# Kernel tuning notes

Measured on AMD Instinct MI355X. Metric: run time of the kernel, lower is better.

## Reference

```python
import jax, jax.numpy as jnp
import numpy as np

N, E, D_NLP, D_EMB = 100000, 500000, 768, 128


def setup_inputs() -> dict:
    key = jax.random.key(0)
    ks = jax.random.split(key, 6)
    z = jax.random.normal(ks[0], (N, D_EMB), jnp.float32)
    z0 = jax.random.normal(ks[1], (N, D_NLP), jnp.float32)
    edge_index = jax.random.randint(ks[2], (2, E), 0, N)
    w0 = jax.random.normal(ks[3], (D_EMB, D_NLP), jnp.float32) / np.sqrt(D_NLP)
    prelu_a = jnp.full((1,), 0.25, jnp.float32)  # torch PReLU default init
    w1 = jax.random.normal(ks[4], (1, 3 * D_EMB), jnp.float32) / np.sqrt(3 * D_EMB)
    b1 = jnp.zeros((1,), jnp.float32)
    return {"z": z, "z0": z0, "edge_index": edge_index, "w0": w0,
            "prelu_a": prelu_a, "w1": w1, "b1": b1}


def reference(z, z0, edge_index, w0, prelu_a, w1, b1):
    # qid = elementwise max of the two endpoint rows, shifted to start at 0
    qid = jnp.max(edge_index[0:2], axis=0)
    qid = qid - qid.min()
    # lin0 (no bias) + PReLU with scalar slope
    h = z0[qid] @ w0.T                       # [E, D_EMB]
    x0 = jnp.where(h >= 0, h, prelu_a[0] * h)
    emb1 = z[edge_index[0]]                  # [E, D_EMB]
    emb2 = z[edge_index[1]]                  # [E, D_EMB]
    # lin1(concat([emb1, emb2, x0])) == sum of three matvecs; avoids a [E, 3*D] concat
    w1a, w1b, w1c = w1[0, :D_EMB], w1[0, D_EMB:2 * D_EMB], w1[0, 2 * D_EMB:]
    out = emb1 @ w1a + emb2 @ w1b + x0 @ w1c + b1[0]
    return out  # [E]
```

## Files before the change

kernel.cpp:

```cpp
#include <hip/hip_runtime.h>
#include <hip/hip_bf16.h>
#include <stdint.h>

#define D_EMB 128
#define D_NLP 768
#define BM 64
#define BK 64
#define NKC (D_NLP / BK)

typedef __attribute__((ext_vector_type(8))) short bf16x8;
typedef __attribute__((ext_vector_type(4))) float f32x4;
typedef __attribute__((ext_vector_type(8))) unsigned short u16x8;

__device__ __forceinline__ unsigned short f2bf(float f) {
  unsigned u = __builtin_bit_cast(unsigned, f);
  u += 0x7fffu + ((u >> 16) & 1u);
  return (unsigned short)(u >> 16);
}

__global__ void kw(const float* __restrict__ w0, unsigned short* __restrict__ w0s,
                   int* __restrict__ mn) {
  if (blockIdx.x == 0 && threadIdx.x == 0) mn[0] = 0x7fffffff;
  int t = blockIdx.x * 256 + threadIdx.x;
  if (t >= (D_EMB * D_NLP) / 8) return;
  int u = t & 7, row = (t >> 3) & 127, kc = t >> 10;
  const float4* src = (const float4*)(w0 + (size_t)row * D_NLP + kc * BK + ((u ^ (row & 7)) * 8));
  float4 v0 = src[0], v1 = src[1];
  u16x8 o;
  o[0] = f2bf(v0.x); o[1] = f2bf(v0.y); o[2] = f2bf(v0.z); o[3] = f2bf(v0.w);
  o[4] = f2bf(v1.x); o[5] = f2bf(v1.y); o[6] = f2bf(v1.z); o[7] = f2bf(v1.w);
  *(u16x8*)(w0s + (size_t)t * 8) = o;
}

__global__ void km(const int* __restrict__ ei, int E, int* __restrict__ mn) {
  int t = blockIdx.x * blockDim.x + threadIdx.x;
  int stride = gridDim.x * blockDim.x;
  int m = 0x7fffffff;
  for (int e = t; e < E; e += stride) {
    int a = ei[e], b = ei[E + e];
    int q = a > b ? a : b;
    m = q < m ? q : m;
  }
  #pragma unroll
  for (int off = 32; off; off >>= 1) {
    int o = __shfl_xor(m, off);
    m = o < m ? o : m;
  }
  if ((threadIdx.x & 63) == 0) atomicMin(mn, m);
}

__global__ __launch_bounds__(256) void kc(
    const float* __restrict__ z0, const float* __restrict__ z,
    const unsigned short* __restrict__ w0s, const float* __restrict__ w1,
    const float* __restrict__ prelu_a, float* __restrict__ sv,
    float* __restrict__ ta, float* __restrict__ tb, int N) {
  __shared__ unsigned short Bb[3][D_EMB * BK];

  const int tid = threadIdx.x;
  const int lane = tid & 63;
  const int wave = tid >> 6;
  const int kg = lane >> 4;
  const int col = lane & 15;
  const int myrow = blockIdx.x * BM + wave * 16 + col;
  const int arow_g = min(myrow, N - 1);
  const float* aBase = z0 + (size_t)arow_g * D_NLP + kg * 8;

  f32x4 acc[8];
  #pragma unroll
  for (int c = 0; c < 8; ++c) acc[c] = (f32x4){0.f, 0.f, 0.f, 0.f};

  float4 fa[3][4];

  auto loadA = [&](int slot, int t) {
    const float4* p0 = (const float4*)(aBase + t * BK);
    const float4* p1 = (const float4*)(aBase + t * BK + 32);
    fa[slot][0] = p0[0]; fa[slot][1] = p0[1];
    fa[slot][2] = p1[0]; fa[slot][3] = p1[1];
  };

  auto stageB = [&](int t, int buf) {
    const unsigned short* g = w0s + (size_t)t * (D_EMB * BK) + (size_t)tid * 8;
    #pragma unroll
    for (int p = 0; p < 4; ++p) {
      __builtin_amdgcn_global_load_lds(
          (const __attribute__((address_space(1))) void*)(g + p * 256 * 8),
          (__attribute__((address_space(3))) void*)&Bb[buf][(wave * 64 + p * 256) * 8],
          16, 0, 0);
    }
  };

  loadA(0, 0); stageB(0, 0);
  loadA(1, 1); stageB(1, 1);

  #pragma unroll
  for (int t = 0; t < NKC; ++t) {
    if (t < NKC - 1) asm volatile("s_waitcnt vmcnt(8)" ::: "memory");
    else             asm volatile("s_waitcnt vmcnt(0)" ::: "memory");
    __builtin_amdgcn_s_barrier();
    if (t + 2 < NKC) {
      loadA((t + 2) % 3, t + 2);
      stageB(t + 2, (t + 2) % 3);
    }
    __builtin_amdgcn_sched_barrier(0);

    const float4* f = fa[t % 3];
    u16x8 v;
    v[0] = f2bf(f[0].x); v[1] = f2bf(f[0].y); v[2] = f2bf(f[0].z); v[3] = f2bf(f[0].w);
    v[4] = f2bf(f[1].x); v[5] = f2bf(f[1].y); v[6] = f2bf(f[1].z); v[7] = f2bf(f[1].w);
    bf16x8 af0 = __builtin_bit_cast(bf16x8, v);
    v[0] = f2bf(f[2].x); v[1] = f2bf(f[2].y); v[2] = f2bf(f[2].z); v[3] = f2bf(f[2].w);
    v[4] = f2bf(f[3].x); v[5] = f2bf(f[3].y); v[6] = f2bf(f[3].z); v[7] = f2bf(f[3].w);
    bf16x8 af1 = __builtin_bit_cast(bf16x8, v);

    const unsigned short* Bbuf = Bb[t % 3];
    #pragma unroll
    for (int ks = 0; ks < 2; ++ks) {
      bf16x8 af = ks == 0 ? af0 : af1;
      #pragma unroll
      for (int c = 0; c < 8; ++c) {
        int brow = c * 16 + col;
        bf16x8 bfr = *(const bf16x8*)&Bbuf[(brow * 8 + ((ks * 4 + kg) ^ (brow & 7))) * 8];
        acc[c] = __builtin_amdgcn_mfma_f32_16x16x32_bf16(af, bfr, acc[c], 0, 0, 0);
      }
    }
  }

  float ap = prelu_a[0];
  float ssum[4] = {0.f, 0.f, 0.f, 0.f};
  #pragma unroll
  for (int c = 0; c < 8; ++c) {
    float wc = w1[2 * D_EMB + c * 16 + col];
    #pragma unroll
    for (int i = 0; i < 4; ++i) {
      float h = acc[c][i];
      float x = h >= 0.f ? h : ap * h;
      ssum[i] += x * wc;
    }
  }
  #pragma unroll
  for (int off = 1; off < 16; off <<= 1) {
    #pragma unroll
    for (int i = 0; i < 4; ++i) ssum[i] += __shfl_xor(ssum[i], off);
  }
  if (col == 0) {
    int rbase = blockIdx.x * BM + wave * 16 + kg * 4;
    #pragma unroll
    for (int i = 0; i < 4; ++i) {
      int r = rbase + i;
      if (r < N) sv[r] = ssum[i];
    }
  }

  {
    const float* zp = z + (size_t)arow_g * D_EMB + kg * 32;
    const float4* wa4 = (const float4*)(w1 + kg * 32);
    const float4* wb4 = (const float4*)(w1 + D_EMB + kg * 32);
    float pa = 0.f, pb = 0.f;
    #pragma unroll
    for (int i = 0; i < 8; ++i) {
      float4 zv = ((const float4*)zp)[i];
      float4 wa = wa4[i];
      float4 wb = wb4[i];
      pa += zv.x * wa.x + zv.y * wa.y + zv.z * wa.z + zv.w * wa.w;
      pb += zv.x * wb.x + zv.y * wb.y + zv.z * wb.z + zv.w * wb.w;
    }
    pa += __shfl_xor(pa, 16); pa += __shfl_xor(pa, 32);
    pb += __shfl_xor(pb, 16); pb += __shfl_xor(pb, 32);
    if (kg == 0 && myrow < N) { ta[myrow] = pa; tb[myrow] = pb; }
  }
}

__global__ void kd(const int* __restrict__ ei, const int* __restrict__ mn,
                   const float* __restrict__ ta, const float* __restrict__ tb,
                   const float* __restrict__ sv, const float* __restrict__ b1,
                   float* __restrict__ out, int E) {
  int e = blockIdx.x * blockDim.x + threadIdx.x;
  if (e >= E) return;
  int i0 = ei[e], i1 = ei[E + e];
  int q = (i0 > i1 ? i0 : i1) - mn[0];
  out[e] = ta[i0] + tb[i1] + sv[q] + b1[0];
}

extern "C" void kernel_launch(void* const* d_in, const int* in_sizes, int n_in,
                              void* d_out, int out_size, void* d_ws, size_t ws_size,
                              hipStream_t stream) {
  const float* z  = (const float*)d_in[0];
  const float* z0 = (const float*)d_in[1];
  const int*   ei = (const int*)d_in[2];
  const float* w0 = (const float*)d_in[3];
  const float* pa = (const float*)d_in[4];
  const float* w1 = (const float*)d_in[5];
  const float* b1 = (const float*)d_in[6];
  float* out = (float*)d_out;
  const int N = in_sizes[0] / D_EMB;
  const int E = in_sizes[2] / 2;

  char* ws = (char*)d_ws;
  int* mn = (int*)ws;
  unsigned short* w0s = (unsigned short*)(ws + 256);
  float* ta = (float*)(ws + 256 + 196608);
  float* tb = ta + N;
  float* sv = tb + N;

  kw<<<(D_EMB * D_NLP / 8 + 255) / 256, 256, 0, stream>>>(w0, w0s, mn);
  km<<<256, 256, 0, stream>>>(ei, E, mn);
  kc<<<(N + BM - 1) / BM, 256, 0, stream>>>(z0, z, w0s, w1, pa, sv, ta, tb, N);
  kd<<<(E + 255) / 256, 256, 0, stream>>>(ei, mn, ta, tb, sv, b1, out, E);
}
```

Measured before the change: 124.8 us.

## Deepen GEMM prefetch pipeline to four stages and use intrinsic bf16 conversion

Raises the multi-buffered pipeline in the z0·w0ᵀ GEMM kernel from three to four stages (LDS B buffers and A register slots), prefetching three K-chunks ahead and adjusting the vmcnt waits. This aims to hide more global-memory latency on the bandwidth-bound z0 stream. It also swaps the manual float-to-bf16 rounding for the __float2bfloat16 intrinsic, which may compile to hardware conversion instructions. The costs are 64 KB of LDS per block instead of 48 KB and 16 more live float4 registers, which can lower occupancy.

```diff
diff --git a/kernel.cpp b/kernel.cpp
--- a/kernel.cpp
+++ b/kernel.cpp
@@ -16,6 +16,19 @@
   unsigned u = __builtin_bit_cast(unsigned, f);
   u += 0x7fffu + ((u >> 16) & 1u);
   return (unsigned short)(u >> 16);
+}
+
+__device__ __forceinline__ bf16x8 pack8(const float4& a, const float4& b) {
+  u16x8 v;
+  v[0] = __builtin_bit_cast(unsigned short, __float2bfloat16(a.x));
+  v[1] = __builtin_bit_cast(unsigned short, __float2bfloat16(a.y));
+  v[2] = __builtin_bit_cast(unsigned short, __float2bfloat16(a.z));
+  v[3] = __builtin_bit_cast(unsigned short, __float2bfloat16(a.w));
+  v[4] = __builtin_bit_cast(unsigned short, __float2bfloat16(b.x));
+  v[5] = __builtin_bit_cast(unsigned short, __float2bfloat16(b.y));
+  v[6] = __builtin_bit_cast(unsigned short, __float2bfloat16(b.z));
+  v[7] = __builtin_bit_cast(unsigned short, __float2bfloat16(b.w));
+  return __builtin_bit_cast(bf16x8, v);
 }
 
 __global__ void kw(const float* __restrict__ w0, unsigned short* __restrict__ w0s,
@@ -54,7 +67,7 @@
     const unsigned short* __restrict__ w0s, const float* __restrict__ w1,
     const float* __restrict__ prelu_a, float* __restrict__ sv,
     float* __restrict__ ta, float* __restrict__ tb, int N) {
-  __shared__ unsigned short Bb[3][D_EMB * BK];
+  __shared__ unsigned short Bb[4][D_EMB * BK];
 
   const int tid = threadIdx.x;
   const int lane = tid & 63;
@@ -69,7 +82,7 @@
   #pragma unroll
   for (int c = 0; c < 8; ++c) acc[c] = (f32x4){0.f, 0.f, 0.f, 0.f};
 
-  float4 fa[3][4];
+  float4 fa[4][4];
 
   auto loadA = [&](int slot, int t) {
     const float4* p0 = (const float4*)(aBase + t * BK);
@@ -91,28 +104,25 @@
 
   loadA(0, 0); stageB(0, 0);
   loadA(1, 1); stageB(1, 1);
+  loadA(2, 2); stageB(2, 2);
 
   #pragma unroll
   for (int t = 0; t < NKC; ++t) {
-    if (t < NKC - 1) asm volatile("s_waitcnt vmcnt(8)" ::: "memory");
-    else             asm volatile("s_waitcnt vmcnt(0)" ::: "memory");
+    if (t <= NKC - 3)      asm volatile("s_waitcnt vmcnt(16)" ::: "memory");
+    else if (t == NKC - 2) asm volatile("s_waitcnt vmcnt(8)" ::: "memory");
+    else                   asm volatile("s_waitcnt vmcnt(0)" ::: "memory");
     __builtin_amdgcn_s_barrier();
-    if (t + 2 < NKC) {
-      loadA((t + 2) % 3, t + 2);
-      stageB(t + 2, (t + 2) % 3);
+    if (t + 3 < NKC) {
+      loadA((t + 3) & 3, t + 3);
+      stageB(t + 3, (t + 3) & 3);
     }
     __builtin_amdgcn_sched_barrier(0);
 
-    const float4* f = fa[t % 3];
-    u16x8 v;
-    v[0] = f2bf(f[0].x); v[1] = f2bf(f[0].y); v[2] = f2bf(f[0].z); v[3] = f2bf(f[0].w);
-    v[4] = f2bf(f[1].x); v[5] = f2bf(f[1].y); v[6] = f2bf(f[1].z); v[7] = f2bf(f[1].w);
-    bf16x8 af0 = __builtin_bit_cast(bf16x8, v);
-    v[0] = f2bf(f[2].x); v[1] = f2bf(f[2].y); v[2] = f2bf(f[2].z); v[3] = f2bf(f[2].w);
-    v[4] = f2bf(f[3].x); v[5] = f2bf(f[3].y); v[6] = f2bf(f[3].z); v[7] = f2bf(f[3].w);
-    bf16x8 af1 = __builtin_bit_cast(bf16x8, v);
-
-    const unsigned short* Bbuf = Bb[t % 3];
+    const float4* f = fa[t & 3];
+    bf16x8 af0 = pack8(f[0], f[1]);
+    bf16x8 af1 = pack8(f[2], f[3]);
+
+    const unsigned short* Bbuf = Bb[t & 3];
     #pragma unroll
     for (int ks = 0; ks < 2; ++ks) {
       bf16x8 af = ks == 0 ? af0 : af1;
```

Result: slower. 130.5 us (+4.6%).
